# Optimization experiments

Measured on AMD Instinct MI355X. Metric: run time of the kernel, lower is better.

The kernel has to match this reference:

```python
import jax, jax.numpy as jnp
import numpy as np

D_MODEL = 1024
N_HEADS = 16
HEAD_DIM = D_MODEL // N_HEADS


def setup_inputs() -> dict:
    key = jax.random.key(0)
    ks = jax.random.split(key, 9)
    s = 1.0 / np.sqrt(D_MODEL)
    inp = {
        "x": jax.random.normal(ks[0], (4, 2048, D_MODEL), dtype=jnp.float32),
        "wq": jax.random.uniform(ks[1], (D_MODEL, D_MODEL), jnp.float32, -s, s),
        "bq": jax.random.uniform(ks[2], (D_MODEL,), jnp.float32, -s, s),
        "wk": jax.random.uniform(ks[3], (D_MODEL, D_MODEL), jnp.float32, -s, s),
        "bk": jax.random.uniform(ks[4], (D_MODEL,), jnp.float32, -s, s),
        "wv": jax.random.uniform(ks[5], (D_MODEL, D_MODEL), jnp.float32, -s, s),
        "bv": jax.random.uniform(ks[6], (D_MODEL,), jnp.float32, -s, s),
        "wo": jax.random.uniform(ks[7], (D_MODEL, D_MODEL), jnp.float32, -s, s),
        "bo": jax.random.uniform(ks[8], (D_MODEL,), jnp.float32, -s, s),
    }
    return inp


def reference(x, wq, bq, wk, bk, wv, bv, wo, bo):
    b, s, d = x.shape
    h, hd = N_HEADS, HEAD_DIM
    # projections (torch Linear: y = x @ W.T + b; here weights stored as [in, out])
    q = (x @ wq + bq).reshape(b, s, h, hd).transpose(0, 2, 1, 3)  # [b,h,s,hd]
    k = (x @ wk + bk).reshape(b, s, h, hd).transpose(0, 2, 1, 3)
    v = (x @ wv + bv).reshape(b, s, h, hd).transpose(0, 2, 1, 3)
    scores = jnp.einsum("bhqd,bhkd->bhqk", q, k) / jnp.sqrt(jnp.float32(hd))
    causal = jnp.tril(jnp.ones((s, s), dtype=bool))
    scores = jnp.where(causal, scores, -jnp.inf)
    weights = jax.nn.softmax(scores, axis=-1)
    attn = jnp.einsum("bhqk,bhkd->bhqd", weights, v)  # [b,h,s,hd]
    attn = attn.transpose(0, 2, 1, 3).reshape(b, s, d)
    return attn @ wo + bo
```

## Files before the change

### kernel.cpp

```cpp
#include <hip/hip_runtime.h>
#include <cstddef>

#define D_MODEL 1024
#define NH 16
#define HD 64
#define BATCH 4
#define SEQ 2048
#define MTOT (BATCH * SEQ)

typedef _Float16 half8 __attribute__((ext_vector_type(8)));
typedef _Float16 half4v __attribute__((ext_vector_type(4)));
typedef float f32x4 __attribute__((ext_vector_type(4)));

#if __has_builtin(__builtin_amdgcn_exp2f)
#define EXP2(x) __builtin_amdgcn_exp2f(x)
#else
#define EXP2(x) __expf((x)*0.69314718056f)
#endif

#define ASYNC_COPY16(g, l)                                                    \
    __builtin_amdgcn_global_load_lds(                                         \
        (__attribute__((address_space(1))) const void*)(g),                   \
        (__attribute__((address_space(3))) void*)(l), 16, 0, 0)

#define LDSFRAG(S, R, CH)                                                     \
    (*(const half8*)((const char*)(S) + ((R) << 7) +                          \
                     ((((CH) << 1)) ^ (((R) & 7) << 4))))

__global__ __launch_bounds__(256) void prep(
    const float* __restrict__ x, _Float16* __restrict__ xh,
    const float* __restrict__ W0, const float* __restrict__ W1,
    const float* __restrict__ W2, const float* __restrict__ W3,
    _Float16* __restrict__ T0, _Float16* __restrict__ T1,
    _Float16* __restrict__ T2, _Float16* __restrict__ T3)
{
    __shared__ float T[64][65];
    const int bid = blockIdx.x;
    if (bid < 256) {
        const size_t base = (size_t)bid * 4096 + threadIdx.x;
#pragma unroll
        for (int it = 0; it < 16; ++it) {
            const size_t i = base + (size_t)it * 256;
            const float4* p = (const float4*)x + 2 * i;
            float4 a = p[0], b = p[1];
            half8 h;
            h[0] = (_Float16)a.x; h[1] = (_Float16)a.y; h[2] = (_Float16)a.z; h[3] = (_Float16)a.w;
            h[4] = (_Float16)b.x; h[5] = (_Float16)b.y; h[6] = (_Float16)b.z; h[7] = (_Float16)b.w;
            *((half8*)xh + i) = h;
        }
    } else {
        const int t = bid - 256;
        const int mtx = t >> 8;
        const float* W = (mtx == 0) ? W0 : (mtx == 1) ? W1 : (mtx == 2) ? W2 : W3;
        _Float16*   Wt = (mtx == 0) ? T0 : (mtx == 1) ? T1 : (mtx == 2) ? T2 : T3;
        const int tile = t & 255;
        const int k0 = (tile >> 4) * 64, n0 = (tile & 15) * 64;
        const int r = threadIdx.x >> 4, c4 = (threadIdx.x & 15) * 4;

#pragma unroll
        for (int i = 0; i < 4; ++i) {
            float4 v = *(const float4*)(W + (size_t)(k0 + r + 16 * i) * 1024 + n0 + c4);
            T[r + 16 * i][c4 + 0] = v.x; T[r + 16 * i][c4 + 1] = v.y;
            T[r + 16 * i][c4 + 2] = v.z; T[r + 16 * i][c4 + 3] = v.w;
        }
        __syncthreads();
#pragma unroll
        for (int i = 0; i < 4; ++i) {
            const int n = r + 16 * i;
            half4v h;
            h[0] = (_Float16)T[c4 + 0][n]; h[1] = (_Float16)T[c4 + 1][n];
            h[2] = (_Float16)T[c4 + 2][n]; h[3] = (_Float16)T[c4 + 3][n];
            *(half4v*)(Wt + (size_t)(n0 + n) * 1024 + k0 + c4) = h;
        }
    }
}

template <int QKV>
__global__ __launch_bounds__(256) void gemm_mfma(
    const _Float16* __restrict__ A,
    const _Float16* __restrict__ Bt0, const _Float16* __restrict__ Bt1, const _Float16* __restrict__ Bt2,
    const float* __restrict__ bi0, const float* __restrict__ bi1, const float* __restrict__ bi2,
    void* __restrict__ C0, void* __restrict__ C1, void* __restrict__ C2)
{
    const int L = blockIdx.x;
    const int y = L & 63;
    const int c_ = L >> 6;
    const int z  = QKV ? (c_ >> 3) : 0;
    const int xb = QKV ? (c_ & 7) : c_;

    const _Float16* Bt = (z == 0) ? Bt0 : (z == 1) ? Bt1 : Bt2;
    const float*   bia = (z == 0) ? bi0 : (z == 1) ? bi1 : bi2;
    void*            C = (z == 0) ? C0  : (z == 1) ? C1  : C2;

    __shared__ _Float16 As[128][64];
    __shared__ _Float16 Bs[128][64];

    const int tid  = threadIdx.x;
    const int w    = tid >> 6;
    const int lane = tid & 63;
    const int l15  = lane & 15;
    const int lg   = lane >> 4;
    const int m0 = y * 128;
    const int n0 = xb * 128;
    const int wm = (w >> 1) * 64, wn = (w & 1) * 64;

    const int rsub = lane >> 3;
    const int cswz = ((lane & 7) ^ rsub) * 8;

    const _Float16* gA = A  + (size_t)(m0 + 32 * w + rsub) * 1024 + cswz;
    const _Float16* gB = Bt + (size_t)(n0 + 32 * w + rsub) * 1024 + cswz;
    char* lA = (char*)As + (size_t)(w * 4) * 1024;
    char* lB = (char*)Bs + (size_t)(w * 4) * 1024;

    f32x4 acc[4][4];
#pragma unroll
    for (int i = 0; i < 4; ++i)
#pragma unroll
        for (int j = 0; j < 4; ++j) { acc[i][j][0] = 0.f; acc[i][j][1] = 0.f; acc[i][j][2] = 0.f; acc[i][j][3] = 0.f; }

    for (int kt = 0; kt < 16; ++kt) {
        const int k0 = kt * 64;
        __syncthreads();
#pragma unroll
        for (int i = 0; i < 4; ++i) {
            ASYNC_COPY16(gA + (size_t)(8 * i) * 1024 + k0, lA + i * 1024);
            ASYNC_COPY16(gB + (size_t)(8 * i) * 1024 + k0, lB + i * 1024);
        }
        __syncthreads();

#pragma unroll
        for (int c = 0; c < 2; ++c) {
            half8 af[4], bf[4];
#pragma unroll
            for (int i = 0; i < 4; ++i) af[i] = LDSFRAG(As, wm + 16 * i + l15, 32 * c + 8 * lg);
#pragma unroll
            for (int j = 0; j < 4; ++j) bf[j] = LDSFRAG(Bs, wn + 16 * j + l15, 32 * c + 8 * lg);
#pragma unroll
            for (int i = 0; i < 4; ++i)
#pragma unroll
                for (int j = 0; j < 4; ++j)
                    acc[i][j] = __builtin_amdgcn_mfma_f32_16x16x32_f16(af[i], bf[j], acc[i][j], 0, 0, 0);
        }
    }

    float bvv[4];
#pragma unroll
    for (int j = 0; j < 4; ++j) bvv[j] = bia[n0 + wn + 16 * j + l15];

#pragma unroll
    for (int i = 0; i < 4; ++i)
#pragma unroll
        for (int j = 0; j < 4; ++j)
#pragma unroll
            for (int r = 0; r < 4; ++r) {
                const int m = m0 + wm + 16 * i + 4 * lg + r;
                const int n = n0 + wn + 16 * j + l15;
                const float val = acc[i][j][r] + bvv[j];
                if (QKV) {
                    const int bb = m >> 11, ss = m & 2047, hh = n >> 6, hd = n & 63;
                    if (z < 2)
                        ((_Float16*)C)[((size_t)(bb * NH + hh) * SEQ + ss) * HD + hd] = (_Float16)val;
                    else
                        ((_Float16*)C)[((size_t)(bb * NH + hh) * HD + hd) * SEQ + ss] = (_Float16)val;
                } else {
                    ((float*)C)[(size_t)m * 1024 + n] = val;
                }
            }
}

__global__ __launch_bounds__(256, 4) void attn_fwd_mfma(
    const _Float16* __restrict__ Q, const _Float16* __restrict__ K,
    const _Float16* __restrict__ Vt, _Float16* __restrict__ O)
{
    __shared__ _Float16 Ks[64][80];
    __shared__ _Float16 Vs[64][80];
    __shared__ _Float16 Ps[4][16][80];

    const int tid  = threadIdx.x;
    const int w    = tid >> 6;
    const int lane = tid & 63;
    const int l15  = lane & 15;
    const int lg   = lane >> 4;

    const int bh = blockIdx.y;
    const int b  = bh >> 4, h = bh & 15;

    const _Float16* Qb  = Q  + (size_t)bh * SEQ * HD;
    const _Float16* Kb  = K  + (size_t)bh * SEQ * HD;
    const _Float16* Vtb = Vt + (size_t)bh * HD * SEQ;

    const int srow = tid >> 3;
    const int scol = (tid & 7) * 8;

    for (int pass = 0; pass < 2; ++pass) {
        const int qt = pass ? (int)blockIdx.x : (31 - (int)blockIdx.x);
        const int q0 = qt * 64;
        const int ntiles = qt + 1;

        half8 qa[2];
        {
            const _Float16* qp = Qb + (size_t)(q0 + 16 * w + l15) * HD + 8 * lg;
            qa[0] = *(const half8*)(qp);
            qa[1] = *(const half8*)(qp + 32);
#pragma unroll
            for (int c = 0; c < 2; ++c)
#pragma unroll
                for (int j = 0; j < 8; ++j)
                    qa[c][j] = (_Float16)((float)qa[c][j] * 0.18033688f);
        }

        f32x4 o_[4];
#pragma unroll
        for (int ft = 0; ft < 4; ++ft) { o_[ft][0] = 0.f; o_[ft][1] = 0.f; o_[ft][2] = 0.f; o_[ft][3] = 0.f; }
        float lp[4] = {0.f, 0.f, 0.f, 0.f};

        half8 kreg[2], vreg[2];
#pragma unroll
        for (int j = 0; j < 2; ++j) {
            kreg[j] = *(const half8*)(Kb  + (size_t)(srow + 32 * j) * HD + scol);
            vreg[j] = *(const half8*)(Vtb + (size_t)(srow + 32 * j) * SEQ + scol);
        }

        for (int kt = 0; kt < ntiles; ++kt) {
            __syncthreads();
#pragma unroll
            for (int j = 0; j < 2; ++j) {
                *(half8*)&Ks[srow + 32 * j][scol] = kreg[j];
                *(half8*)&Vs[srow + 32 * j][scol] = vreg[j];
            }
            __syncthreads();

            if (kt + 1 < ntiles) {
                const int k0 = (kt + 1) * 64;
#pragma unroll
                for (int j = 0; j < 2; ++j) {
                    kreg[j] = *(const half8*)(Kb  + (size_t)(k0 + srow + 32 * j) * HD + scol);
                    vreg[j] = *(const half8*)(Vtb + (size_t)(srow + 32 * j) * SEQ + k0 + scol);
                }
            }

            f32x4 s[4];
#pragma unroll
            for (int f = 0; f < 4; ++f) { s[f][0] = 0.f; s[f][1] = 0.f; s[f][2] = 0.f; s[f][3] = 0.f; }
#pragma unroll
            for (int c = 0; c < 2; ++c)
#pragma unroll
                for (int f = 0; f < 4; ++f) {
                    half8 kb = *(const half8*)&Ks[16 * f + l15][32 * c + 8 * lg];
                    s[f] = __builtin_amdgcn_mfma_f32_16x16x32_f16(qa[c], kb, s[f], 0, 0, 0);
                }

            const bool dg = (kt == qt);
#pragma unroll
            for (int f = 0; f < 4; ++f)
#pragma unroll
                for (int r = 0; r < 4; ++r) {
                    float p = EXP2(s[f][r]);
                    if (dg && (16 * f + l15 > 16 * w + 4 * lg + r)) p = 0.f;
                    lp[r] += p;
                    Ps[w][4 * lg + r][16 * f + l15] = (_Float16)p;
                }

            half8 pa[2];
            pa[0] = *(const half8*)&Ps[w][l15][8 * lg];
            pa[1] = *(const half8*)&Ps[w][l15][32 + 8 * lg];
#pragma unroll
            for (int c = 0; c < 2; ++c)
#pragma unroll
                for (int ft = 0; ft < 4; ++ft) {
                    half8 vb = *(const half8*)&Vs[16 * ft + l15][32 * c + 8 * lg];
                    o_[ft] = __builtin_amdgcn_mfma_f32_16x16x32_f16(pa[c], vb, o_[ft], 0, 0, 0);
                }
        }

#pragma unroll
        for (int r = 0; r < 4; ++r) {
            float rs = lp[r];
            rs += __shfl_xor(rs, 1);
            rs += __shfl_xor(rs, 2);
            rs += __shfl_xor(rs, 4);
            rs += __shfl_xor(rs, 8);
            const float inv = 1.0f / rs;
            _Float16* orow = O + (size_t)(b * SEQ + q0 + 16 * w + 4 * lg + r) * D_MODEL + h * HD + l15;
#pragma unroll
            for (int ft = 0; ft < 4; ++ft) orow[16 * ft] = (_Float16)(o_[ft][r] * inv);
        }
        __syncthreads();
    }
}

extern "C" void kernel_launch(void* const* d_in, const int* in_sizes, int n_in,
                              void* d_out, int out_size, void* d_ws, size_t ws_size,
                              hipStream_t stream)
{
    const float* x  = (const float*)d_in[0];
    const float* wq = (const float*)d_in[1];
    const float* bq = (const float*)d_in[2];
    const float* wk = (const float*)d_in[3];
    const float* bk = (const float*)d_in[4];
    const float* wv = (const float*)d_in[5];
    const float* bv = (const float*)d_in[6];
    const float* wo = (const float*)d_in[7];
    const float* bo = (const float*)d_in[8];
    float* out = (float*)d_out;

    const size_t SZ = (size_t)MTOT * D_MODEL;
    const size_t WZ = (size_t)D_MODEL * D_MODEL;

    _Float16* xh  = (_Float16*)d_ws;
    _Float16* wtq = xh + SZ;
    _Float16* wtk = wtq + WZ;
    _Float16* wtv = wtk + WZ;
    _Float16* wto = wtv + WZ;
    _Float16* Qh  = wto + WZ;
    _Float16* Kh  = Qh + SZ;
    _Float16* Vtg = Kh + SZ;
    _Float16* AOh = Vtg + SZ;

    prep<<<dim3(1280), 256, 0, stream>>>(x, xh, wq, wk, wv, wo, wtq, wtk, wtv, wto);
    gemm_mfma<1><<<dim3(1536), 256, 0, stream>>>(xh, wtq, wtk, wtv, bq, bk, bv, Qh, Kh, Vtg);
    attn_fwd_mfma<<<dim3(16, BATCH * NH), 256, 0, stream>>>(Qh, Kh, Vtg, AOh);
    gemm_mfma<0><<<dim3(512), 256, 0, stream>>>(AOh, wto, wto, wto, bo, bo, bo, out, out, out);
}
```

Before: 269.3 us.

## Rewrite projection GEMM as 256x256 tile, 8-wave, double-buffered pipelined MFMA kernel

```diff
diff --git a/kernel.cpp b/kernel.cpp
--- a/kernel.cpp
+++ b/kernel.cpp
@@ -76,71 +76,126 @@
 }
 
 template <int QKV>
-__global__ __launch_bounds__(256) void gemm_mfma(
+__global__ __launch_bounds__(512, 2) void gemm_mfma(
     const _Float16* __restrict__ A,
     const _Float16* __restrict__ Bt0, const _Float16* __restrict__ Bt1, const _Float16* __restrict__ Bt2,
     const float* __restrict__ bi0, const float* __restrict__ bi1, const float* __restrict__ bi2,
     void* __restrict__ C0, void* __restrict__ C1, void* __restrict__ C2)
 {
+    constexpr int NT = 16;
+    __shared__ _Float16 As[2][256][64];
+    __shared__ _Float16 Bs[2][256][64];
+
     const int L = blockIdx.x;
-    const int y = L & 63;
-    const int c_ = L >> 6;
-    const int z  = QKV ? (c_ >> 3) : 0;
-    const int xb = QKV ? (c_ & 7) : c_;
+    int y, z, xb;
+    if (QKV) {
+        const int wg = (L & 7) * 48 + (L >> 3);
+        y = wg / 12;
+        const int cn = wg % 12;
+        z = cn >> 2; xb = cn & 3;
+    } else {
+        const int wg = (L & 7) * 16 + (L >> 3);
+        y = wg >> 2; z = 0; xb = wg & 3;
+    }
 
     const _Float16* Bt = (z == 0) ? Bt0 : (z == 1) ? Bt1 : Bt2;
     const float*   bia = (z == 0) ? bi0 : (z == 1) ? bi1 : bi2;
     void*            C = (z == 0) ? C0  : (z == 1) ? C1  : C2;
-
-    __shared__ _Float16 As[128][64];
-    __shared__ _Float16 Bs[128][64];
 
     const int tid  = threadIdx.x;
     const int w    = tid >> 6;
     const int lane = tid & 63;
     const int l15  = lane & 15;
     const int lg   = lane >> 4;
-    const int m0 = y * 128;
-    const int n0 = xb * 128;
-    const int wm = (w >> 1) * 64, wn = (w & 1) * 64;
+    const int m0 = y * 256;
+    const int n0 = xb * 256;
+    const int wm = (w >> 2) * 128;
+    const int wn = (w & 3) * 64;
 
     const int rsub = lane >> 3;
-    const int cswz = ((lane & 7) ^ rsub) * 8;
-
-    const _Float16* gA = A  + (size_t)(m0 + 32 * w + rsub) * 1024 + cswz;
-    const _Float16* gB = Bt + (size_t)(n0 + 32 * w + rsub) * 1024 + cswz;
-    char* lA = (char*)As + (size_t)(w * 4) * 1024;
-    char* lB = (char*)Bs + (size_t)(w * 4) * 1024;
-
-    f32x4 acc[4][4];
-#pragma unroll
-    for (int i = 0; i < 4; ++i)
+    const int csw  = ((lane & 7) ^ rsub) * 8;
+    const _Float16* gA = A  + (size_t)(m0 + rsub) * 1024 + csw;
+    const _Float16* gB = Bt + (size_t)(n0 + rsub) * 1024 + csw;
+
+#define STAGE_A(kt_, mh_) do { const int _t = (kt_); if (_t < NT) {           \
+        const size_t _k0 = (size_t)_t * 64;                                   \
+        _Pragma("unroll") for (int _i = 0; _i < 2; ++_i) {                    \
+            const int _c = 2 * w + _i;                                        \
+            const int _r = _c * 8 + ((_c & 8) ? 64 : 0) + (mh_) * 64;         \
+            ASYNC_COPY16(gA + (size_t)_r * 1024 + _k0, &As[_t & 1][_r][0]);   \
+        } } } while (0)
+#define STAGE_B(kt_, nh_) do { const int _t = (kt_); if (_t < NT) {           \
+        const size_t _k0 = (size_t)_t * 64;                                   \
+        _Pragma("unroll") for (int _i = 0; _i < 2; ++_i) {                    \
+            const int _c = 2 * w + _i;                                        \
+            const int _r = (_c >> 2) * 64 + (nh_) * 32 + (_c & 3) * 8;        \
+            ASYNC_COPY16(gB + (size_t)_r * 1024 + _k0, &Bs[_t & 1][_r][0]);   \
+        } } } while (0)
+#define READ_A(mh_) do {                                                      \
+        _Pragma("unroll") for (int _q = 0; _q < 4; ++_q)                      \
+        _Pragma("unroll") for (int _kk = 0; _kk < 2; ++_kk)                   \
+            af[_q][_kk] = LDSFRAG(&As[cur][0][0],                             \
+                wm + 16 * (4 * (mh_) + _q) + l15, 32 * _kk + 8 * lg);         \
+    } while (0)
+#define READ_B(nh_) do {                                                      \
+        _Pragma("unroll") for (int _p = 0; _p < 2; ++_p)                      \
+        _Pragma("unroll") for (int _kk = 0; _kk < 2; ++_kk)                   \
+            bf[_p][_kk] = LDSFRAG(&Bs[cur][0][0],                             \
+                wn + 16 * (2 * (nh_) + _p) + l15, 32 * _kk + 8 * lg);         \
+    } while (0)
+#define DO_MFMA(mh_, nh_) do {                                                \
+        __builtin_amdgcn_s_setprio(1);                                        \
+        _Pragma("unroll") for (int _q = 0; _q < 4; ++_q)                      \
+        _Pragma("unroll") for (int _p = 0; _p < 2; ++_p)                      \
+        _Pragma("unroll") for (int _kk = 0; _kk < 2; ++_kk)                   \
+            acc[4 * (mh_) + _q][2 * (nh_) + _p] =                             \
+                __builtin_amdgcn_mfma_f32_16x16x32_f16(                       \
+                    af[_q][_kk], bf[_p][_kk],                                 \
+                    acc[4 * (mh_) + _q][2 * (nh_) + _p], 0, 0, 0);            \
+        __builtin_amdgcn_s_setprio(0);                                        \
+    } while (0)
+#define BARS() do { __builtin_amdgcn_s_barrier();                             \
+        __builtin_amdgcn_sched_barrier(0); } while (0)
+#define WAITLGKM() do { asm volatile("s_waitcnt lgkmcnt(0)" ::: "memory");    \
+        __builtin_amdgcn_sched_barrier(0); } while (0)
+#define WAITVM(n_) do { asm volatile("s_waitcnt vmcnt(" #n_ ")" ::: "memory");\
+        __builtin_amdgcn_sched_barrier(0); } while (0)
+
+    STAGE_A(0, 1);
+    STAGE_B(0, 1);
+    STAGE_A(0, 0);
+    STAGE_B(0, 0);
+    STAGE_A(1, 0);
+    STAGE_B(1, 1);
+
+    f32x4 acc[8][4];
+#pragma unroll
+    for (int i = 0; i < 8; ++i)
 #pragma unroll
         for (int j = 0; j < 4; ++j) { acc[i][j][0] = 0.f; acc[i][j][1] = 0.f; acc[i][j][2] = 0.f; acc[i][j][3] = 0.f; }
 
-    for (int kt = 0; kt < 16; ++kt) {
-        const int k0 = kt * 64;
-        __syncthreads();
-#pragma unroll
-        for (int i = 0; i < 4; ++i) {
-            ASYNC_COPY16(gA + (size_t)(8 * i) * 1024 + k0, lA + i * 1024);
-            ASYNC_COPY16(gB + (size_t)(8 * i) * 1024 + k0, lB + i * 1024);
-        }
-        __syncthreads();
-
-#pragma unroll
-        for (int c = 0; c < 2; ++c) {
-            half8 af[4], bf[4];
-#pragma unroll
-            for (int i = 0; i < 4; ++i) af[i] = LDSFRAG(As, wm + 16 * i + l15, 32 * c + 8 * lg);
-#pragma unroll
-            for (int j = 0; j < 4; ++j) bf[j] = LDSFRAG(Bs, wn + 16 * j + l15, 32 * c + 8 * lg);
-#pragma unroll
-            for (int i = 0; i < 4; ++i)
-#pragma unroll
-                for (int j = 0; j < 4; ++j)
-                    acc[i][j] = __builtin_amdgcn_mfma_f32_16x16x32_f16(af[i], bf[j], acc[i][j], 0, 0, 0);
-        }
+    half8 af[4][2], bf[2][2];
+
+    WAITVM(4);
+    BARS();
+
+#pragma unroll 1
+    for (int kt = 0; kt < NT; ++kt) {
+        const int cur = kt & 1;
+        READ_A(0); READ_B(0);
+        STAGE_A(kt + 1, 1);
+        BARS(); WAITLGKM(); DO_MFMA(0, 0); BARS();
+        READ_B(1);
+        STAGE_B(kt + 1, 0);
+        BARS(); WAITLGKM(); DO_MFMA(0, 1); BARS();
+        READ_A(1);
+        STAGE_A(kt + 2, 0);
+        BARS(); WAITLGKM(); DO_MFMA(1, 1); BARS();
+        READ_B(0);
+        STAGE_B(kt + 2, 1);
+        if (kt < NT - 2) WAITVM(4);
+        else             WAITVM(0);
+        BARS(); WAITLGKM(); DO_MFMA(1, 0); BARS();
     }
 
     float bvv[4];
@@ -148,7 +203,7 @@
     for (int j = 0; j < 4; ++j) bvv[j] = bia[n0 + wn + 16 * j + l15];
 
 #pragma unroll
-    for (int i = 0; i < 4; ++i)
+    for (int i = 0; i < 8; ++i)
 #pragma unroll
         for (int j = 0; j < 4; ++j)
 #pragma unroll
@@ -166,6 +221,14 @@
                     ((float*)C)[(size_t)m * 1024 + n] = val;
                 }
             }
+#undef STAGE_A
+#undef STAGE_B
+#undef READ_A
+#undef READ_B
+#undef DO_MFMA
+#undef BARS
+#undef WAITLGKM
+#undef WAITVM
 }
 
 __global__ __launch_bounds__(256, 4) void attn_fwd_mfma(
@@ -318,7 +381,7 @@
     _Float16* AOh = Vtg + SZ;
 
     prep<<<dim3(1280), 256, 0, stream>>>(x, xh, wq, wk, wv, wo, wtq, wtk, wtv, wto);
-    gemm_mfma<1><<<dim3(1536), 256, 0, stream>>>(xh, wtq, wtk, wtv, bq, bk, bv, Qh, Kh, Vtg);
+    gemm_mfma<1><<<dim3(384), 512, 0, stream>>>(xh, wtq, wtk, wtv, bq, bk, bv, Qh, Kh, Vtg);
     attn_fwd_mfma<<<dim3(16, BATCH * NH), 256, 0, stream>>>(Qh, Kh, Vtg, AOh);
-    gemm_mfma<0><<<dim3(512), 256, 0, stream>>>(AOh, wto, wto, wto, bo, bo, bo, out, out, out);
+    gemm_mfma<0><<<dim3(128), 512, 0, stream>>>(AOh, wto, wto, wto, bo, bo, bo, out, out, out);
 }
```

Measured after the change: 292.5 us. +8.6%, slower.

## Double-buffer attention K/V tiles with async global-to-LDS copies and XOR swizzle

Applied to the files above, without the earlier changes.

```diff
diff --git a/kernel.cpp b/kernel.cpp
--- a/kernel.cpp
+++ b/kernel.cpp
@@ -168,12 +168,12 @@
             }
 }
 
-__global__ __launch_bounds__(256, 4) void attn_fwd_mfma(
+__global__ __launch_bounds__(256, 3) void attn_fwd_mfma(
     const _Float16* __restrict__ Q, const _Float16* __restrict__ K,
     const _Float16* __restrict__ Vt, _Float16* __restrict__ O)
 {
-    __shared__ _Float16 Ks[64][80];
-    __shared__ _Float16 Vs[64][80];
+    __shared__ _Float16 Ks[2][64][64];
+    __shared__ _Float16 Vs[2][64][64];
     __shared__ _Float16 Ps[4][16][80];
 
     const int tid  = threadIdx.x;
@@ -189,13 +189,20 @@
     const _Float16* Kb  = K  + (size_t)bh * SEQ * HD;
     const _Float16* Vtb = Vt + (size_t)bh * HD * SEQ;
 
-    const int srow = tid >> 3;
-    const int scol = (tid & 7) * 8;
+    const int rsub = lane >> 3;
+    const int cswz = ((lane & 7) ^ rsub) * 8;
 
     for (int pass = 0; pass < 2; ++pass) {
         const int qt = pass ? (int)blockIdx.x : (31 - (int)blockIdx.x);
         const int q0 = qt * 64;
         const int ntiles = qt + 1;
+
+#pragma unroll
+        for (int i = 0; i < 2; ++i) {
+            const int c = 2 * w + i;
+            ASYNC_COPY16(Kb  + (size_t)(c * 8 + rsub) * HD  + cswz, &Ks[0][c * 8][0]);
+            ASYNC_COPY16(Vtb + (size_t)(c * 8 + rsub) * SEQ + cswz, &Vs[0][c * 8][0]);
+        }
 
         half8 qa[2];
         {
@@ -214,28 +221,20 @@
         for (int ft = 0; ft < 4; ++ft) { o_[ft][0] = 0.f; o_[ft][1] = 0.f; o_[ft][2] = 0.f; o_[ft][3] = 0.f; }
         float lp[4] = {0.f, 0.f, 0.f, 0.f};
 
-        half8 kreg[2], vreg[2];
-#pragma unroll
-        for (int j = 0; j < 2; ++j) {
-            kreg[j] = *(const half8*)(Kb  + (size_t)(srow + 32 * j) * HD + scol);
-            vreg[j] = *(const half8*)(Vtb + (size_t)(srow + 32 * j) * SEQ + scol);
-        }
-
         for (int kt = 0; kt < ntiles; ++kt) {
-            __syncthreads();
-#pragma unroll
-            for (int j = 0; j < 2; ++j) {
-                *(half8*)&Ks[srow + 32 * j][scol] = kreg[j];
-                *(half8*)&Vs[srow + 32 * j][scol] = vreg[j];
-            }
-            __syncthreads();
+            const int cur = kt & 1;
+            asm volatile("s_waitcnt vmcnt(0)" ::: "memory");
+            __builtin_amdgcn_s_barrier();
 
             if (kt + 1 < ntiles) {
                 const int k0 = (kt + 1) * 64;
 #pragma unroll
-                for (int j = 0; j < 2; ++j) {
-                    kreg[j] = *(const half8*)(Kb  + (size_t)(k0 + srow + 32 * j) * HD + scol);
-                    vreg[j] = *(const half8*)(Vtb + (size_t)(srow + 32 * j) * SEQ + k0 + scol);
+                for (int i = 0; i < 2; ++i) {
+                    const int c = 2 * w + i;
+                    ASYNC_COPY16(Kb  + (size_t)(k0 + c * 8 + rsub) * HD + cswz,
+                                 &Ks[cur ^ 1][c * 8][0]);
+                    ASYNC_COPY16(Vtb + (size_t)(c * 8 + rsub) * SEQ + k0 + cswz,
+                                 &Vs[cur ^ 1][c * 8][0]);
                 }
             }
 
@@ -246,7 +245,7 @@
             for (int c = 0; c < 2; ++c)
 #pragma unroll
                 for (int f = 0; f < 4; ++f) {
-                    half8 kb = *(const half8*)&Ks[16 * f + l15][32 * c + 8 * lg];
+                    half8 kb = LDSFRAG(&Ks[cur][0][0], 16 * f + l15, 32 * c + 8 * lg);
                     s[f] = __builtin_amdgcn_mfma_f32_16x16x32_f16(qa[c], kb, s[f], 0, 0, 0);
                 }
 
@@ -268,7 +267,7 @@
             for (int c = 0; c < 2; ++c)
 #pragma unroll
                 for (int ft = 0; ft < 4; ++ft) {
-                    half8 vb = *(const half8*)&Vs[16 * ft + l15][32 * c + 8 * lg];
+                    half8 vb = LDSFRAG(&Vs[cur][0][0], 16 * ft + l15, 32 * c + 8 * lg);
                     o_[ft] = __builtin_amdgcn_mfma_f32_16x16x32_f16(pa[c], vb, o_[ft], 0, 0, 0);
                 }
         }
```

Result: slower. 284.2 us (+5.5%).
